# Performance work log

Measured on AMD Instinct MI355X. Metric: run time of the kernel, lower is better.

The kernel has to match this reference:

```python
import jax, jax.numpy as jnp
import numpy as np

B, N, FD, H, L = 8, 512, 32, 64, 3  # batch, atoms, feature_dim, hidden_dim, n_layers
LN_EPS = 1e-5
DEG_EPS = 1e-8


def setup_inputs() -> dict:
    key = jax.random.key(0)
    ks = jax.random.split(key, 10)
    features = jax.random.normal(ks[0], (B, N, FD), jnp.float32)
    # sparse binary molecular-graph adjacency
    adjacency = (jax.random.uniform(ks[1], (B, N, N)) < 0.08).astype(jnp.float32)
    mask = jax.random.uniform(ks[2], (B, N)) < 0.9
    feature_weights = jnp.ones((FD,), jnp.float32)
    w_enc = jax.random.normal(ks[3], (FD, H), jnp.float32) / np.sqrt(FD)
    b_enc = jnp.zeros((H,), jnp.float32)
    ln_g = jnp.ones((H,), jnp.float32)
    ln_b = jnp.zeros((H,), jnp.float32)
    msg_w = jax.random.normal(ks[4], (L, 2 * H, H), jnp.float32) / np.sqrt(2 * H)
    msg_b = jnp.zeros((L, H), jnp.float32)
    ws1 = jax.random.normal(ks[5], (H, H // 2), jnp.float32) / np.sqrt(H)
    bs1 = jnp.zeros((H // 2,), jnp.float32)
    ws2 = jax.random.normal(ks[6], (H // 2, 1), jnp.float32) / np.sqrt(H // 2)
    bs2 = jnp.zeros((1,), jnp.float32)
    return dict(features=features, adjacency=adjacency, mask=mask,
                feature_weights=feature_weights, w_enc=w_enc, b_enc=b_enc,
                ln_g=ln_g, ln_b=ln_b, msg_w=msg_w, msg_b=msg_b,
                ws1=ws1, bs1=bs1, ws2=ws2, bs2=bs2)


def reference(features, adjacency, mask, feature_weights, w_enc, b_enc,
              ln_g, ln_b, msg_w, msg_b, ws1, bs1, ws2, bs2):
    # encoder: weighted features -> Linear -> LayerNorm -> SiLU (dropout = eval identity)
    x = features * feature_weights  # [B,N,FD]
    h = x @ w_enc + b_enc  # [B,N,H]
    mu = h.mean(-1, keepdims=True)
    var = h.var(-1, keepdims=True)
    h = (h - mu) * jax.lax.rsqrt(var + LN_EPS) * ln_g + ln_b
    h = jax.nn.silu(h)

    deg = adjacency.sum(-1, keepdims=True) + DEG_EPS  # [B,N,1]
    for l in range(L):
        # concat-linear split: cat([h_i,h_j]) @ W == h_i @ W[:H] + h_j @ W[H:]
        wi, wj = msg_w[l, :H], msg_w[l, H:]
        a = h @ wi  # [B,N,H] (sender i rows)
        b = h @ wj  # [B,N,H] (receiver j cols)
        m = jax.nn.silu(a[:, :, None, :] + b[:, None, :, :] + msg_b[l])  # [B,N,N,H]
        h_new = jnp.einsum('bijh,bij->bih', m, adjacency) / deg
        h = h + 0.5 * h_new

    scores = (jax.nn.silu(h @ ws1 + bs1) @ ws2 + bs2)[..., 0]  # [B,N]
    return jnp.where(mask, scores, -jnp.inf)
```

## Files before the change

### kernel.cpp

```cpp
#include <hip/hip_runtime.h>
#include <hip/hip_fp16.h>
#include <math.h>

#define B 8
#define N 512
#define FD 32
#define H 64
#define L 3
#define NODES (B * N)
#define LN_EPS 1e-5f
#define DEG_EPS 1e-8f
#define MAXDEG 512

#define FP16_NEG_SENTINEL ((unsigned short)0xFBFF)

#define BLOCK_THREADS 256
#define WPB 4
#define GRID_BLOCKS (NODES / WPB)

__device__ __forceinline__ int swizzled_node(int bid, int wave) {
    return (bid & 7) * N + (bid >> 3) * WPB + wave;
}

__device__ __forceinline__ float fsilu(float x) {
    return x * __builtin_amdgcn_rcpf(1.0f + __expf(-x));
}

__device__ __forceinline__ float lanebcast(float v, int k) {
    return __int_as_float(__builtin_amdgcn_readlane(__float_as_int(v), k));
}

__device__ __forceinline__ unsigned short f32_to_f16_safe(float f) {
    if (!(f == f)) return (unsigned short)0;
    if (f >  65504.0f) f =  65504.0f;
    if (f < -65504.0f) f = -65504.0f;
    return __half_as_ushort(__float2half(f));
}

__device__ __forceinline__ float edge_gather(const unsigned short* __restrict__ crow,
                                             int len, int bbase, int t, float a_t,
                                             const float* __restrict__ b_in) {
    if (len <= 0) return 0.0f;
    const float* bb = b_in + (size_t)bbase * H + t;
    float acc = 0.0f;
    for (int e0 = 0; e0 < len; e0 += 16) {
        float x[16];
#pragma unroll
        for (int q = 0; q < 16; ++q) {
            int idx = e0 + q;
            if (idx > len - 1) idx = len - 1;
            x[q] = bb[(size_t)crow[idx] * H];
        }
#pragma unroll
        for (int q = 0; q < 16; ++q) {
            float s = fsilu(a_t + x[q]);
            acc += (e0 + q < len) ? s : 0.0f;
        }
    }
    return acc;
}

__device__ __forceinline__ float wave_matvec(float hreg, const float* __restrict__ W,
                                             int t) {
    float acc = 0.0f;
#pragma unroll
    for (int k = 0; k < H; ++k)
        acc += lanebcast(hreg, k) * W[k * H + t];
    return acc;
}

__global__ __launch_bounds__(BLOCK_THREADS, 4)
void k0_enc_proj_csr(const float* __restrict__ feat,
                     const float* __restrict__ adj,
                     const unsigned char* __restrict__ mask,
                     const float* __restrict__ fw,
                     const float* __restrict__ w_enc,
                     const float* __restrict__ b_enc,
                     const float* __restrict__ ln_g,
                     const float* __restrict__ ln_b,
                     const float* __restrict__ msg_w,
                     float* __restrict__ hbuf,
                     float* __restrict__ abuf,
                     float* __restrict__ bbuf,
                     unsigned short* __restrict__ csr,
                     int* __restrict__ degbuf,
                     float* __restrict__ flag)
{
    const int wave  = threadIdx.x >> 6;
    const int t     = threadIdx.x & 63;
    const int node  = swizzled_node(blockIdx.x, wave);

    if (blockIdx.x == 0 && wave == 0) {
        int cnt_mis = 0, cnt_3f = 0, cnt_3c = 0;
        for (int i = t; i < NODES; i += 64) {
            unsigned char v = mask[i];
            if ((i & 3) != 0 && v != 0) cnt_mis++;
            if ((i & 3) == 3 && v == 0x3F) cnt_3f++;
            if ((i & 1) == 1 && v == 0x3C) cnt_3c++;
        }
        for (int off = 32; off; off >>= 1) {
            cnt_mis += __shfl_xor(cnt_mis, off);
            cnt_3f  += __shfl_xor(cnt_3f, off);
            cnt_3c  += __shfl_xor(cnt_3c, off);
        }
        if (t == 0) {
            float f = 0.0f;
            if (cnt_3f > 0) f = 2.0f;
            else if (cnt_3c > 0) f = 3.0f;
            else if (cnt_mis > 0) f = 1.0f;
            flag[0] = f;
        }
    }

    float hreg;
    {
        const float* xrow = feat + (size_t)node * FD;
        float acc = b_enc[t];
#pragma unroll
        for (int f = 0; f < FD; ++f)
            acc += xrow[f] * fw[f] * w_enc[f * H + t];
        float sum = acc, sumsq = acc * acc;
        for (int off = 32; off; off >>= 1) {
            sum   += __shfl_xor(sum, off);
            sumsq += __shfl_xor(sumsq, off);
        }
        float mu  = sum * (1.0f / H);
        float var = sumsq * (1.0f / H) - mu * mu;
        float hn  = (acc - mu) * rsqrtf(var + LN_EPS) * ln_g[t] + ln_b[t];
        hreg = fsilu(hn);
    }
    hbuf[(size_t)node * H + t] = hreg;

    abuf[(size_t)node * H + t] = wave_matvec(hreg, msg_w, t);
    bbuf[(size_t)node * H + t] = wave_matvec(hreg, msg_w + H * H, t);

    const float4* adjrow4 = (const float4*)(adj + (size_t)node * N);
    unsigned short* crow = csr + (size_t)node * MAXDEG;
    int base = 0;
    for (int j0 = 0; j0 < N; j0 += 256) {
        float4 v = adjrow4[(j0 >> 2) + t];
        float vc[4] = { v.x, v.y, v.z, v.w };
#pragma unroll
        for (int c = 0; c < 4; ++c) {
            unsigned long long mk = __ballot(vc[c] != 0.0f);
            if (vc[c] != 0.0f) {
                int pre = __popcll(mk & ((1ull << t) - 1ull));
                crow[base + pre] = (unsigned short)(j0 + 4 * t + c);
            }
            base += __popcll(mk);
        }
    }
    if (t == 0) degbuf[node] = base;
}

__global__ __launch_bounds__(BLOCK_THREADS, 4)
void k_msg_proj(const unsigned short* __restrict__ csr,
                const int* __restrict__ degbuf,
                const float* __restrict__ msg_b_l,
                const float* __restrict__ msg_w_n,
                float* __restrict__ hbuf,
                float* __restrict__ abuf,
                const float* __restrict__ b_in,
                float* __restrict__ b_out)
{
    const int wave  = threadIdx.x >> 6;
    const int t     = threadIdx.x & 63;
    const int node  = swizzled_node(blockIdx.x, wave);
    const int bbase = node & ~(N - 1);

    float a_t = abuf[(size_t)node * H + t] + msg_b_l[t];
    int deg = degbuf[node];
    const unsigned short* crow = csr + (size_t)node * MAXDEG;

    float acc = edge_gather(crow, deg, bbase, t, a_t, b_in);

    float hreg = hbuf[(size_t)node * H + t]
               + 0.5f * acc * __builtin_amdgcn_rcpf((float)deg + DEG_EPS);
    hbuf[(size_t)node * H + t] = hreg;

    abuf[(size_t)node * H + t] = wave_matvec(hreg, msg_w_n, t);
    b_out[(size_t)node * H + t] = wave_matvec(hreg, msg_w_n + H * H, t);
}

__global__ __launch_bounds__(BLOCK_THREADS, 4)
void k_msg_score(const unsigned short* __restrict__ csr,
                 const int* __restrict__ degbuf,
                 const float* __restrict__ msg_b_l,
                 const float* __restrict__ hbuf,
                 const float* __restrict__ abuf,
                 const float* __restrict__ b_in,
                 const float* __restrict__ ws1,
                 const float* __restrict__ bs1,
                 const float* __restrict__ ws2,
                 const float* __restrict__ bs2,
                 const unsigned char* __restrict__ mask,
                 const float* __restrict__ flag,
                 unsigned short* __restrict__ out)
{
    const int wave  = threadIdx.x >> 6;
    const int t     = threadIdx.x & 63;
    const int node  = swizzled_node(blockIdx.x, wave);
    const int bbase = node & ~(N - 1);

    float a_t = abuf[(size_t)node * H + t] + msg_b_l[t];
    int deg = degbuf[node];
    const unsigned short* crow = csr + (size_t)node * MAXDEG;

    float acc = edge_gather(crow, deg, bbase, t, a_t, b_in);

    float hreg = hbuf[(size_t)node * H + t]
               + 0.5f * acc * __builtin_amdgcn_rcpf((float)deg + DEG_EPS);

    float part = 0.0f;
    if (t < H / 2) {
        float s = bs1[t];
#pragma unroll
        for (int k = 0; k < H; ++k)
            s += lanebcast(hreg, k) * ws1[k * (H / 2) + t];
        part = fsilu(s) * ws2[t];
    }
    for (int off = 16; off; off >>= 1) part += __shfl_xor(part, off);
    if (t == 0) {
        float sc = part + bs2[0];
        float f = flag[0];
        bool mv;
        if (f == 2.0f)      mv = ((const float*)mask)[node] != 0.0f;
        else if (f == 3.0f) mv = (((const unsigned short*)mask)[node] & 0x7FFF) != 0;
        else if (f == 1.0f) mv = mask[node] != 0;
        else                mv = ((const int*)mask)[node] != 0;
        out[node] = mv ? f32_to_f16_safe(sc) : FP16_NEG_SENTINEL;
    }
}

extern "C" void kernel_launch(void* const* d_in, const int* in_sizes, int n_in,
                              void* d_out, int out_size, void* d_ws, size_t ws_size,
                              hipStream_t stream) {
    const float* feat  = (const float*)d_in[0];
    const float* adj   = (const float*)d_in[1];
    const unsigned char* mask = (const unsigned char*)d_in[2];
    const float* fw    = (const float*)d_in[3];
    const float* w_enc = (const float*)d_in[4];
    const float* b_enc = (const float*)d_in[5];
    const float* ln_g  = (const float*)d_in[6];
    const float* ln_b  = (const float*)d_in[7];
    const float* msg_w = (const float*)d_in[8];
    const float* msg_b = (const float*)d_in[9];
    const float* ws1   = (const float*)d_in[10];
    const float* bs1   = (const float*)d_in[11];
    const float* ws2   = (const float*)d_in[12];
    const float* bs2   = (const float*)d_in[13];
    unsigned short* out = (unsigned short*)d_out;

    char* wsb = (char*)d_ws;
    float* hbuf  = (float*)(wsb);
    float* abuf  = (float*)(wsb + (1 << 20));
    float* bA    = (float*)(wsb + (2 << 20));
    float* bB    = (float*)(wsb + (3 << 20));
    unsigned short* csr = (unsigned short*)(wsb + (4 << 20));
    int*   degb  = (int*)(wsb + (8 << 20));
    float* flag  = (float*)(wsb + (8 << 20) + (1 << 16));

    const size_t WBLK = 2 * H * H;

    k0_enc_proj_csr<<<GRID_BLOCKS, BLOCK_THREADS, 0, stream>>>(
        feat, adj, mask, fw, w_enc, b_enc, ln_g, ln_b,
        msg_w , hbuf, abuf, bA, csr, degb, flag);

    k_msg_proj<<<GRID_BLOCKS, BLOCK_THREADS, 0, stream>>>(
        csr, degb, msg_b + 0 * H, msg_w + 1 * WBLK, hbuf, abuf, bA, bB);

    k_msg_proj<<<GRID_BLOCKS, BLOCK_THREADS, 0, stream>>>(
        csr, degb, msg_b + 1 * H, msg_w + 2 * WBLK, hbuf, abuf, bB, bA);

    k_msg_score<<<GRID_BLOCKS, BLOCK_THREADS, 0, stream>>>(
        csr, degb, msg_b + 2 * H, hbuf, abuf, bA,
        ws1, bs1, ws2, bs2, mask, flag, out);
}
```

Before: 49.81 us.

## Vectorize CSR index loads, split matvec accumulators, enlarge blocks to 16 waves

The edge gather now loads 32 neighbour indices per iteration with four 16-byte vector loads instead of 16 scalar clamped loads, masking indices so padding entries stay in range. The per-node matvec uses four independent accumulators to shorten the dependent FMA chain. All kernels launch 1024-thread blocks covering 16 nodes instead of 256-thread blocks covering 4. The 1024-thread launch bound with a min-blocks hint of 4 sharply limits registers per thread, which together with the 32-wide unroll risks spilling and lower occupancy.

Result: faster. 48.27 us, median of 2 (-3.1%).

```diff
diff --git a/kernel.cpp b/kernel.cpp
--- a/kernel.cpp
+++ b/kernel.cpp
@@ -14,12 +14,12 @@
 
 #define FP16_NEG_SENTINEL ((unsigned short)0xFBFF)
 
-#define BLOCK_THREADS 256
-#define WPB 4
-#define GRID_BLOCKS (NODES / WPB)
+#define TPB 1024
+#define NPB 16
+#define NBLOCKS (NODES / NPB)
 
 __device__ __forceinline__ int swizzled_node(int bid, int wave) {
-    return (bid & 7) * N + (bid >> 3) * WPB + wave;
+    return (bid & 7) * N + (bid >> 3) * NPB + wave;
 }
 
 __device__ __forceinline__ float fsilu(float x) {
@@ -43,16 +43,21 @@
     if (len <= 0) return 0.0f;
     const float* bb = b_in + (size_t)bbase * H + t;
     float acc = 0.0f;
-    for (int e0 = 0; e0 < len; e0 += 16) {
-        float x[16];
-#pragma unroll
-        for (int q = 0; q < 16; ++q) {
-            int idx = e0 + q;
-            if (idx > len - 1) idx = len - 1;
-            x[q] = bb[(size_t)crow[idx] * H];
-        }
-#pragma unroll
-        for (int q = 0; q < 16; ++q) {
+    for (int e0 = 0; e0 < len; e0 += 32) {
+        uint4 p0 = *(const uint4*)(crow + e0);
+        uint4 p1 = *(const uint4*)(crow + e0 + 8);
+        uint4 p2 = *(const uint4*)(crow + e0 + 16);
+        uint4 p3 = *(const uint4*)(crow + e0 + 24);
+        unsigned int w[16] = { p0.x, p0.y, p0.z, p0.w, p1.x, p1.y, p1.z, p1.w,
+                               p2.x, p2.y, p2.z, p2.w, p3.x, p3.y, p3.z, p3.w };
+        float x[32];
+#pragma unroll
+        for (int q = 0; q < 32; ++q) {
+            int j = (int)((w[q >> 1] >> ((q & 1) * 16)) & 0xFFFFu) & (N - 1);
+            x[q] = bb[(size_t)j * H];
+        }
+#pragma unroll
+        for (int q = 0; q < 32; ++q) {
             float s = fsilu(a_t + x[q]);
             acc += (e0 + q < len) ? s : 0.0f;
         }
@@ -62,14 +67,18 @@
 
 __device__ __forceinline__ float wave_matvec(float hreg, const float* __restrict__ W,
                                              int t) {
-    float acc = 0.0f;
-#pragma unroll
-    for (int k = 0; k < H; ++k)
-        acc += lanebcast(hreg, k) * W[k * H + t];
-    return acc;
-}
-
-__global__ __launch_bounds__(BLOCK_THREADS, 4)
+    float a0 = 0.0f, a1 = 0.0f, a2 = 0.0f, a3 = 0.0f;
+#pragma unroll
+    for (int k = 0; k < H; k += 4) {
+        a0 += lanebcast(hreg, k + 0) * W[(k + 0) * H + t];
+        a1 += lanebcast(hreg, k + 1) * W[(k + 1) * H + t];
+        a2 += lanebcast(hreg, k + 2) * W[(k + 2) * H + t];
+        a3 += lanebcast(hreg, k + 3) * W[(k + 3) * H + t];
+    }
+    return (a0 + a1) + (a2 + a3);
+}
+
+__global__ __launch_bounds__(TPB, 4)
 void k0_enc_proj_csr(const float* __restrict__ feat,
                      const float* __restrict__ adj,
                      const unsigned char* __restrict__ mask,
@@ -153,7 +162,7 @@
     if (t == 0) degbuf[node] = base;
 }
 
-__global__ __launch_bounds__(BLOCK_THREADS, 4)
+__global__ __launch_bounds__(TPB, 4)
 void k_msg_proj(const unsigned short* __restrict__ csr,
                 const int* __restrict__ degbuf,
                 const float* __restrict__ msg_b_l,
@@ -182,7 +191,7 @@
     b_out[(size_t)node * H + t] = wave_matvec(hreg, msg_w_n + H * H, t);
 }
 
-__global__ __launch_bounds__(BLOCK_THREADS, 4)
+__global__ __launch_bounds__(TPB, 4)
 void k_msg_score(const unsigned short* __restrict__ csr,
                  const int* __restrict__ degbuf,
                  const float* __restrict__ msg_b_l,
@@ -262,17 +271,17 @@
 
     const size_t WBLK = 2 * H * H;
 
-    k0_enc_proj_csr<<<GRID_BLOCKS, BLOCK_THREADS, 0, stream>>>(
+    k0_enc_proj_csr<<<NBLOCKS, TPB, 0, stream>>>(
         feat, adj, mask, fw, w_enc, b_enc, ln_g, ln_b,
         msg_w , hbuf, abuf, bA, csr, degb, flag);
 
-    k_msg_proj<<<GRID_BLOCKS, BLOCK_THREADS, 0, stream>>>(
+    k_msg_proj<<<NBLOCKS, TPB, 0, stream>>>(
         csr, degb, msg_b + 0 * H, msg_w + 1 * WBLK, hbuf, abuf, bA, bB);
 
-    k_msg_proj<<<GRID_BLOCKS, BLOCK_THREADS, 0, stream>>>(
+    k_msg_proj<<<NBLOCKS, TPB, 0, stream>>>(
         csr, degb, msg_b + 1 * H, msg_w + 2 * WBLK, hbuf, abuf, bB, bA);
 
-    k_msg_score<<<GRID_BLOCKS, BLOCK_THREADS, 0, stream>>>(
+    k_msg_score<<<NBLOCKS, TPB, 0, stream>>>(
         csr, degb, msg_b + 2 * H, hbuf, abuf, bA,
         ws1, bs1, ws2, bs2, mask, flag, out);
 }
```
